# Performance work log

Measured on AMD Instinct MI355X. Metric: run time of the kernel, lower is better.

## Reference

```python
import jax, jax.numpy as jnp
import numpy as np

V, D, S, L, DK, DV, H, B = 32000, 1024, 1024, 4, 64, 64, 16, 4
DFF = 4 * D
EPS = 1e-5


def setup_inputs() -> dict:
    key = jax.random.key(0)
    ks = jax.random.split(key, 20)
    s = 0.02
    n = jax.random.normal
    return {
        "idx": jax.random.randint(ks[0], (B, S), 0, V, dtype=jnp.int32),
        "tok_emb": n(ks[1], (V, D), jnp.float32) * s,
        "pos_emb": n(ks[2], (S, D), jnp.float32) * s,
        "wq": n(ks[3], (L, H, D, DK), jnp.float32) * s,
        "wk": n(ks[4], (L, H, D, DK), jnp.float32) * s,
        "wv": n(ks[5], (L, H, D, DV), jnp.float32) * s,
        "wo": n(ks[6], (L, H * DV, D), jnp.float32) * s,
        "w1": n(ks[7], (L, D, DFF), jnp.float32) * s,
        "b1": jnp.zeros((L, DFF), jnp.float32),
        "w2": n(ks[8], (L, DFF, D), jnp.float32) * s,
        "b2": jnp.zeros((L, D), jnp.float32),
        "ln1_g": jnp.ones((L, D), jnp.float32),
        "ln1_b": jnp.zeros((L, D), jnp.float32),
        "ln2_g": jnp.ones((L, D), jnp.float32),
        "ln2_b": jnp.zeros((L, D), jnp.float32),
        "lnf_g": jnp.ones((D,), jnp.float32),
        "lnf_b": jnp.zeros((D,), jnp.float32),
        "lm_w": n(ks[9], (D, V), jnp.float32) * s,
        "lm_b": jnp.zeros((V,), jnp.float32),
    }


def _ln(x, g, b):
    mu = jnp.mean(x, axis=-1, keepdims=True)
    var = jnp.mean(jnp.square(x - mu), axis=-1, keepdims=True)
    return (x - mu) * jax.lax.rsqrt(var + EPS) * g + b


def _gpt(idx, tok_emb, pos_emb, wq, wk, wv, wo, w1, b1, w2, b2,
         ln1_g, ln1_b, ln2_g, ln2_b, lnf_g, lnf_b, lm_w, lm_b):
    x = tok_emb[idx] + pos_emb[None, :, :]          # [B,S,D]
    causal = jnp.tril(jnp.ones((S, S), bool))        # tril mask buffer
    scale = 1.0 / jnp.sqrt(jnp.asarray(DK, x.dtype))

    def block(x, p):
        wq, wk, wv, wo, w1, b1, w2, b2, g1, be1, g2, be2 = p
        h = _ln(x, g1, be1)
        Q = jnp.einsum('bsd,hdk->bhsk', h, wq)
        K = jnp.einsum('bsd,hdk->bhsk', h, wk)
        Vv = jnp.einsum('bsd,hdv->bhsv', h, wv)
        att = jnp.einsum('bhsk,bhtk->bhst', Q, K) * scale
        att = jnp.where(causal, att, -jnp.inf)
        att = jax.nn.softmax(att, axis=-1)
        o = jnp.einsum('bhst,bhtv->bshv', att, Vv).reshape(x.shape[0], S, H * DV)
        x = x + o @ wo
        h2 = _ln(x, g2, be2)
        x = x + jax.nn.relu(h2 @ w1 + b1) @ w2 + be2 * 0 + b2
        return x, None

    x, _ = jax.lax.scan(block, x, (wq, wk, wv, wo, w1, b1, w2, b2,
                                   ln1_g, ln1_b, ln2_g, ln2_b))
    x = _ln(x, lnf_g, lnf_b)
    logits = x @ lm_w + lm_b                          # [B,S,V]
    return logits


def reference(idx, tok_emb, pos_emb, wq, wk, wv, wo, w1, b1, w2, b2,
              ln1_g, ln1_b, ln2_g, ln2_b, lnf_g, lnf_b, lm_w, lm_b):
    return _gpt(idx, tok_emb, pos_emb, wq, wk, wv, wo, w1, b1, w2, b2,
                ln1_g, ln1_b, ln2_g, ln2_b, lnf_g, lnf_b, lm_w, lm_b)
```

## Files before the change

### kernel.cpp

```cpp
#include <hip/hip_runtime.h>
#include <hip/hip_bf16.h>

#define V_   32000
#define VP_  32768
#define D_   1024
#define S_   1024
#define L_   4
#define H_   16
#define B_   4
#define DFF_ 4096
#define M_   (B_*S_)

using bf_t = __hip_bfloat16;
typedef __bf16 bf16x8 __attribute__((ext_vector_type(8)));
typedef __bf16 bf16x4 __attribute__((ext_vector_type(4)));
typedef float  f32x4  __attribute__((ext_vector_type(4)));

#define AS1(p) ((__attribute__((address_space(1))) void*)(p))
#define AS3(p) ((__attribute__((address_space(3))) void*)(p))

__global__ __launch_bounds__(256) void k_transpose_bf16(
    const float* __restrict__ src, bf_t* __restrict__ dst,
    int R, int C, long srcS1, long srcS2, long dstS1, long dstS2, int n2)
{
  const int z  = blockIdx.z;
  const int z1 = z / n2, z2 = z % n2;
  src += (size_t)z1 * srcS1 + (size_t)z2 * srcS2;
  dst += (size_t)z1 * dstS1 + (size_t)z2 * dstS2;
  __shared__ float tile[32][33];
  const int c0 = blockIdx.x * 32, r0 = blockIdx.y * 32;
  const int lx = threadIdx.x, ly = threadIdx.y;
  #pragma unroll
  for (int i = 0; i < 32; i += 8)
    tile[ly + i][lx] = src[(size_t)(r0 + ly + i) * C + (c0 + lx)];
  __syncthreads();
  #pragma unroll
  for (int i = 0; i < 32; i += 8)
    dst[(size_t)(c0 + ly + i) * R + (r0 + lx)] = __float2bfloat16(tile[lx][ly + i]);
}

__global__ __launch_bounds__(256) void k_embed(
    const int* __restrict__ idx, const float* __restrict__ tok,
    const float* __restrict__ pos, float* __restrict__ x)
{
  const int row = blockIdx.x;
  const int s   = row & (S_ - 1);
  const int t   = idx[row];
  const float4* tr = (const float4*)(tok + (size_t)t * D_);
  const float4* pr = (const float4*)(pos + (size_t)s * D_);
  float4* xr = (float4*)(x + (size_t)row * D_);
  const int i = threadIdx.x;
  float4 a = tr[i], b = pr[i];
  xr[i] = make_float4(a.x + b.x, a.y + b.y, a.z + b.z, a.w + b.w);
}

__global__ __launch_bounds__(256) void k_ln(
    const float* __restrict__ x, const float* __restrict__ g,
    const float* __restrict__ bb, bf_t* __restrict__ out)
{
  __shared__ float red[8];
  const int row = blockIdx.x, tid = threadIdx.x;
  const float4 v = ((const float4*)(x + (size_t)row * D_))[tid];
  float s = v.x + v.y + v.z + v.w;
  #pragma unroll
  for (int o = 32; o > 0; o >>= 1) s += __shfl_down(s, o);
  if ((tid & 63) == 0) red[tid >> 6] = s;
  __syncthreads();
  const float mu = (red[0] + red[1] + red[2] + red[3]) * (1.f / D_);
  const float dx = v.x - mu, dy = v.y - mu, dz = v.z - mu, dw = v.w - mu;
  float ss = dx*dx + dy*dy + dz*dz + dw*dw;
  #pragma unroll
  for (int o = 32; o > 0; o >>= 1) ss += __shfl_down(ss, o);
  if ((tid & 63) == 0) red[4 + (tid >> 6)] = ss;
  __syncthreads();
  const float var = (red[4] + red[5] + red[6] + red[7]) * (1.f / D_);
  const float rs  = rsqrtf(var + 1e-5f);
  const float4 gv = ((const float4*)g)[tid];
  const float4 bv = ((const float4*)bb)[tid];
  const size_t base = (size_t)row * D_ + tid * 4;
  out[base + 0] = __float2bfloat16(dx * rs * gv.x + bv.x);
  out[base + 1] = __float2bfloat16(dy * rs * gv.y + bv.y);
  out[base + 2] = __float2bfloat16(dz * rs * gv.z + bv.z);
  out[base + 3] = __float2bfloat16(dw * rs * gv.w + bv.w);
}

__global__ __launch_bounds__(256) void k_combine_ln(
    float* __restrict__ x, const float* __restrict__ P, long pstride,
    const float* __restrict__ cbias,
    const float* __restrict__ g, const float* __restrict__ bb,
    bf_t* __restrict__ out)
{
  __shared__ float red[8];
  const int row = blockIdx.x, tid = threadIdx.x;
  const size_t i = (size_t)row * 256 + tid;
  float4 a = ((const float4*)x)[i];
  {
    const float4 p0 = ((const float4*)P)[i];
    const float4 p1 = ((const float4*)(P + pstride))[i];
    a.x += p0.x + p1.x; a.y += p0.y + p1.y;
    a.z += p0.z + p1.z; a.w += p0.w + p1.w;
  }
  if (cbias) {
    const float4 bv = ((const float4*)cbias)[tid];
    a.x += bv.x; a.y += bv.y; a.z += bv.z; a.w += bv.w;
  }
  ((float4*)x)[i] = a;
  float s = a.x + a.y + a.z + a.w;
  #pragma unroll
  for (int o = 32; o > 0; o >>= 1) s += __shfl_down(s, o);
  if ((tid & 63) == 0) red[tid >> 6] = s;
  __syncthreads();
  const float mu = (red[0] + red[1] + red[2] + red[3]) * (1.f / D_);
  const float dx = a.x - mu, dy = a.y - mu, dz = a.z - mu, dw = a.w - mu;
  float ss = dx*dx + dy*dy + dz*dz + dw*dw;
  #pragma unroll
  for (int o = 32; o > 0; o >>= 1) ss += __shfl_down(ss, o);
  if ((tid & 63) == 0) red[4 + (tid >> 6)] = ss;
  __syncthreads();
  const float var = (red[4] + red[5] + red[6] + red[7]) * (1.f / D_);
  const float rs  = rsqrtf(var + 1e-5f);
  const float4 gv = ((const float4*)g)[tid];
  const float4 bv = ((const float4*)bb)[tid];
  const size_t base = (size_t)row * D_ + tid * 4;
  out[base + 0] = __float2bfloat16(dx * rs * gv.x + bv.x);
  out[base + 1] = __float2bfloat16(dy * rs * gv.y + bv.y);
  out[base + 2] = __float2bfloat16(dz * rs * gv.z + bv.z);
  out[base + 3] = __float2bfloat16(dw * rs * gv.w + bv.w);
}

template<bool HAS_BIAS, bool RELU, bool OUT_BF16, bool NT, int PARTS>
__global__ __launch_bounds__(256) void k_gemm(
    const bf_t* __restrict__ A, const bf_t* __restrict__ Bt,
    float* outF, bf_t* outB,
    const float* __restrict__ bias,
    int N, int ld, int Klen, long pstride)
{
  __shared__ __bf16 As[2][128 * 64];
  __shared__ __bf16 Bs[2][128 * 64];
  const int tid  = threadIdx.x;
  const int lane = tid & 63, wid = tid >> 6;
  int bp = blockIdx.x, kh = 0;
  if (PARTS > 1) { const int T = gridDim.x / PARTS; kh = bp / T; bp %= T; }
  const int i  = bp >> 3;
  const int nt = (bp & 7) + 8 * (i >> 5);
  const int mt = i & 31;
  const int m0 = mt * 128;
  const int n0 = nt * 128;
  if (n0 >= N) return;
  const int kb = kh * Klen;
  f32x4 acc[4][4] = {};

  const int srow = lane >> 3;
  const int scol = ((lane & 7) ^ (lane >> 3)) * 8;
  const int mw = (wid >> 1) * 64, nw = (wid & 1) * 64;
  const int NTk = Klen >> 6;

  #pragma unroll
  for (int i2 = 0; i2 < 4; ++i2) {
    const int chunk = i2 * 4 + wid;
    const int r = chunk * 8 + srow;
    __builtin_amdgcn_global_load_lds(AS1(A  + (size_t)(m0 + r) * ld + kb + scol),
                                     AS3(&As[0][chunk * 512]), 16, 0, 0);
    __builtin_amdgcn_global_load_lds(AS1(Bt + (size_t)(n0 + r) * ld + kb + scol),
                                     AS3(&Bs[0][chunk * 512]), 16, 0, 0);
  }

  for (int t = 0; t < NTk; ++t) {
    __syncthreads();
    if (t + 1 < NTk) {
      const int kt = (t + 1) << 6;
      #pragma unroll
      for (int i2 = 0; i2 < 4; ++i2) {
        const int chunk = i2 * 4 + wid;
        const int r = chunk * 8 + srow;
        __builtin_amdgcn_global_load_lds(AS1(A  + (size_t)(m0 + r) * ld + kb + kt + scol),
                                         AS3(&As[(t + 1) & 1][chunk * 512]), 16, 0, 0);
        __builtin_amdgcn_global_load_lds(AS1(Bt + (size_t)(n0 + r) * ld + kb + kt + scol),
                                         AS3(&Bs[(t + 1) & 1][chunk * 512]), 16, 0, 0);
      }
    }
    const __bf16* Ab = As[t & 1];
    const __bf16* Bb = Bs[t & 1];
    #pragma unroll
    for (int kk = 0; kk < 2; ++kk) {
      const int ck = kk * 4 + (lane >> 4);
      bf16x8 af[4], bfr[4];
      #pragma unroll
      for (int mi = 0; mi < 4; ++mi) {
        const int r = mw + mi * 16 + (lane & 15);
        af[mi] = *(const bf16x8*)&Ab[r * 64 + ((ck ^ (r & 7)) * 8)];
      }
      #pragma unroll
      for (int ni = 0; ni < 4; ++ni) {
        const int r = nw + ni * 16 + (lane & 15);
        bfr[ni] = *(const bf16x8*)&Bb[r * 64 + ((ck ^ (r & 7)) * 8)];
      }
      #pragma unroll
      for (int mi = 0; mi < 4; ++mi)
        #pragma unroll
        for (int ni = 0; ni < 4; ++ni)
          acc[mi][ni] = __builtin_amdgcn_mfma_f32_16x16x32_bf16(af[mi], bfr[ni], acc[mi][ni], 0, 0, 0);
    }
  }

  float* outP = outF + (PARTS > 1 ? (size_t)kh * pstride : 0);
  const int cr = (lane >> 4) * 4, cc = lane & 15;
  #pragma unroll
  for (int mi = 0; mi < 4; ++mi) {
    #pragma unroll
    for (int ni = 0; ni < 4; ++ni) {
      const int col = n0 + nw + ni * 16 + cc;
      const float bv = HAS_BIAS ? bias[col] : 0.f;
      #pragma unroll
      for (int j = 0; j < 4; ++j) {
        const int row = m0 + mw + mi * 16 + cr + j;
        float v = acc[mi][ni][j] + bv;
        if (RELU)  v = fmaxf(v, 0.f);
        if (OUT_BF16) {
          outB[(size_t)row * N + col] = __float2bfloat16(v);
        } else if (NT) {
          __builtin_nontemporal_store(v, &outP[(size_t)row * N + col]);
        } else {
          outP[(size_t)row * N + col] = v;
        }
      }
    }
  }
}

__device__ __forceinline__ void stage256(
    const bf_t* __restrict__ A, const bf_t* __restrict__ Bt,
    int m0, int n0, int lda, int kt, int wid, int lane, __bf16* buf)
{
  #pragma unroll
  for (int p = 0; p < 4; ++p) {
    const int sb   = p * 512 + wid * 64;
    const int slot = sb + lane;
    const int row  = slot >> 3;
    const int c    = (slot & 7) ^ (row & 7);
    __builtin_amdgcn_global_load_lds(AS1(A  + (size_t)(m0 + row) * lda + kt + c * 8),
                                     AS3(buf + sb * 8), 16, 0, 0);
    __builtin_amdgcn_global_load_lds(AS1(Bt + (size_t)(n0 + row) * lda + kt + c * 8),
                                     AS3(buf + 16384 + sb * 8), 16, 0, 0);
  }
}

template<bool HAS_BIAS, bool RELU, bool OUT_BF16, bool NT, int MAP>
__global__ __launch_bounds__(512, 2) void k_gemm256(
    const bf_t* __restrict__ A, const bf_t* __restrict__ Bt,
    float* outF, bf_t* outB, const float* __restrict__ bias,
    int N, int Nvalid, int K)
{
  __shared__ __align__(16) __bf16 LDS[65536];
  const int tid = threadIdx.x, lane = tid & 63, wid = tid >> 6;
  int mt, nt;
  if (MAP == 0) { mt = blockIdx.x & 15; nt = blockIdx.x >> 4; }
  else {
    const int xcd = blockIdx.x & 7, i = blockIdx.x >> 3;
    mt = i & 15; nt = xcd + 8 * (i >> 4);
  }
  const int m0 = mt * 256, n0 = nt * 256;
  if (n0 >= Nvalid) return;
  const int wm = wid >> 2, wn = wid & 3;
  const int l4 = lane & 15, lhi = lane >> 4;

  f32x4 acc[8][4] = {};
  const int NTILES = K >> 6;

  stage256(A, Bt, m0, n0, K, 0,  wid, lane, LDS);
  stage256(A, Bt, m0, n0, K, 64, wid, lane, LDS + 32768);

  for (int t = 0; t < NTILES; ++t) {
    __bf16* buf = LDS + (t & 1) * 32768;
    if (t < NTILES - 1) asm volatile("s_waitcnt vmcnt(8)" ::: "memory");
    else                asm volatile("s_waitcnt vmcnt(0)" ::: "memory");
    __builtin_amdgcn_s_barrier();
    asm volatile("" ::: "memory");

    bf16x8 bq[4][2];
    #pragma unroll
    for (int ni = 0; ni < 4; ++ni) {
      const int r = wn * 64 + ni * 16 + l4;
      bq[ni][0] = *(const bf16x8*)&buf[16384 + r * 64 + ((lhi ^ (r & 7)) * 8)];
      bq[ni][1] = *(const bf16x8*)&buf[16384 + r * 64 + (((4 + lhi) ^ (r & 7)) * 8)];
    }
    bf16x8 aq[2][2][2];
    #pragma unroll
    for (int mi = 0; mi < 2; ++mi) {
      const int r = wm * 128 + mi * 16 + l4;
      aq[0][mi][0] = *(const bf16x8*)&buf[r * 64 + ((lhi ^ (r & 7)) * 8)];
      aq[0][mi][1] = *(const bf16x8*)&buf[r * 64 + (((4 + lhi) ^ (r & 7)) * 8)];
    }
    #pragma unroll
    for (int q = 0; q < 4; ++q) {
      if (q < 3) {
        #pragma unroll
        for (int mi = 0; mi < 2; ++mi) {
          const int r = wm * 128 + ((q + 1) * 2 + mi) * 16 + l4;
          aq[(q + 1) & 1][mi][0] = *(const bf16x8*)&buf[r * 64 + ((lhi ^ (r & 7)) * 8)];
          aq[(q + 1) & 1][mi][1] = *(const bf16x8*)&buf[r * 64 + (((4 + lhi) ^ (r & 7)) * 8)];
        }
      }
      #pragma unroll
      for (int mi = 0; mi < 2; ++mi)
        #pragma unroll
        for (int ni = 0; ni < 4; ++ni) {
          acc[q * 2 + mi][ni] = __builtin_amdgcn_mfma_f32_16x16x32_bf16(
              aq[q & 1][mi][0], bq[ni][0], acc[q * 2 + mi][ni], 0, 0, 0);
          acc[q * 2 + mi][ni] = __builtin_amdgcn_mfma_f32_16x16x32_bf16(
              aq[q & 1][mi][1], bq[ni][1], acc[q * 2 + mi][ni], 0, 0, 0);
        }
    }

    asm volatile("s_waitcnt lgkmcnt(0)" ::: "memory");
    __builtin_amdgcn_sched_barrier(0);
    __builtin_amdgcn_s_barrier();
    if (t + 2 < NTILES)
      stage256(A, Bt, m0, n0, K, (t + 2) * 64, wid, lane, buf);
  }

  float* slab = (float*)LDS + wid * 1088;
  float bval[4];
  if (HAS_BIAS) {
    #pragma unroll
    for (int ni = 0; ni < 4; ++ni) bval[ni] = bias[n0 + wn * 64 + ni * 16 + l4];
  }
  #pragma unroll
  for (int mi = 0; mi < 8; ++mi) {
    #pragma unroll
    for (int ni = 0; ni < 4; ++ni)
      #pragma unroll
      for (int j = 0; j < 4; ++j) {
        float v = acc[mi][ni][j];
        if (HAS_BIAS) v += bval[ni];
        if (RELU) v = fmaxf(v, 0.f);
        slab[(lhi * 4 + j) * 68 + ni * 16 + l4] = v;
      }
    const int grow0 = m0 + wm * 128 + mi * 16;
    const int ncol0 = n0 + wn * 64;
    #pragma unroll
    for (int q = 0; q < 4; ++q) {
      const int r16 = q * 4 + lhi;
      const f32x4 v = *(const f32x4*)&slab[r16 * 68 + l4 * 4];
      const size_t gaddr = (size_t)(grow0 + r16) * N + ncol0 + l4 * 4;
      if (OUT_BF16) {
        bf16x4 o4;
        o4[0] = (__bf16)v[0]; o4[1] = (__bf16)v[1];
        o4[2] = (__bf16)v[2]; o4[3] = (__bf16)v[3];
        *(bf16x4*)(outB + gaddr) = o4;
      } else if (NT) {
        __builtin_nontemporal_store(v, (f32x4*)(outF + gaddr));
      } else {
        *(f32x4*)(outF + gaddr) = v;
      }
    }
  }
}

__global__ __launch_bounds__(256) void k_attn_mfma(
    const bf_t* __restrict__ qkv, bf_t* __restrict__ o)
{
  __shared__ __bf16 Qs[64 * 64];
  __shared__ __bf16 Ks[64 * 64];
  __shared__ __bf16 Vt[64 * 64];
  __shared__ __bf16 Ps[4][16 * 64];

  const int qt = blockIdx.x, bh = blockIdx.y;
  const int b = bh >> 4, h = bh & 15;
  const int tid = threadIdx.x, lane = tid & 63, wid = tid >> 6;
  const int qbase = qt * 64;
  const int r0 = wid * 16;
  const int l4 = lane & 15, lhi = lane >> 4;

  #pragma unroll
  for (int p = 0; p < 2; ++p) {
    const int idx = p * 256 + tid;
    const int r = idx >> 3, c8 = idx & 7;
    const bf16x8 v = *(const bf16x8*)(qkv + (size_t)(b * S_ + qbase + r) * 3072 + h * 64 + c8 * 8);
    *(bf16x8*)&Qs[r * 64 + ((c8 ^ (r & 7)) * 8)] = v;
  }

  f32x4 oa[4];
  #pragma unroll
  for (int di = 0; di < 4; ++di) oa[di] = (f32x4){0.f, 0.f, 0.f, 0.f};
  float mrow = -1e30f, lrow = 0.f;

  const float SCL = 0.125f * 1.44269504089f;

  for (int kt = 0; kt <= qt; ++kt) {
    __syncthreads();
    #pragma unroll
    for (int p = 0; p < 2; ++p) {
      const int idx = p * 256 + tid;
      const int r = idx >> 3, c8 = idx & 7;
      const size_t gbase = (size_t)(b * S_ + kt * 64 + r) * 3072 + h * 64 + c8 * 8;
      const bf16x8 kv = *(const bf16x8*)(qkv + gbase + 1024);
      *(bf16x8*)&Ks[r * 64 + ((c8 ^ (r & 7)) * 8)] = kv;
      const bf16x8 vv = *(const bf16x8*)(qkv + gbase + 2048);
      #pragma unroll
      for (int i = 0; i < 8; ++i) {
        const int d = c8 * 8 + i;
        Vt[d * 64 + (((r >> 3) ^ i ^ c8) * 8) + (r & 7)] = vv[i];
      }
    }
    __syncthreads();

    f32x4 s[4];
    #pragma unroll
    for (int ni = 0; ni < 4; ++ni) s[ni] = (f32x4){0.f, 0.f, 0.f, 0.f};
    const int qr = r0 + l4;
    __builtin_amdgcn_s_setprio(1);
    #pragma unroll
    for (int kk = 0; kk < 2; ++kk) {
      const int ck = kk * 4 + lhi;
      const bf16x8 bq = *(const bf16x8*)&Qs[qr * 64 + ((ck ^ (qr & 7)) * 8)];
      #pragma unroll
      for (int ni = 0; ni < 4; ++ni) {
        const int t = ni * 16 + l4;
        const bf16x8 ak = *(const bf16x8*)&Ks[t * 64 + ((ck ^ (t & 7)) * 8)];
        s[ni] = __builtin_amdgcn_mfma_f32_16x16x32_bf16(ak, bq, s[ni], 0, 0, 0);
      }
    }
    __builtin_amdgcn_s_setprio(0);

    #pragma unroll
    for (int ni = 0; ni < 4; ++ni)
      #pragma unroll
      for (int j = 0; j < 4; ++j)
        s[ni][j] *= SCL;
    if (kt == qt) {
      #pragma unroll
      for (int ni = 0; ni < 4; ++ni)
        #pragma unroll
        for (int j = 0; j < 4; ++j)
          if (ni * 16 + lhi * 4 + j > r0 + l4) s[ni][j] = -1e30f;
    }

    float mloc = -1e30f;
    #pragma unroll
    for (int ni = 0; ni < 4; ++ni)
      #pragma unroll
      for (int j = 0; j < 4; ++j) mloc = fmaxf(mloc, s[ni][j]);
    mloc = fmaxf(mloc, __shfl_xor(mloc, 16));
    mloc = fmaxf(mloc, __shfl_xor(mloc, 32));
    float cscale = 1.f;
    if (!__all(mloc <= mrow + 8.f)) {
      const float mnew = fmaxf(mrow, mloc);
      cscale = exp2f(mrow - mnew);
      #pragma unroll
      for (int j = 0; j < 4; ++j) {
        const float cj = __shfl(cscale, lhi * 4 + j);
        #pragma unroll
        for (int di = 0; di < 4; ++di) oa[di][j] *= cj;
      }
      mrow = mnew;
    }
    float ssum = 0.f;
    #pragma unroll
    for (int ni = 0; ni < 4; ++ni)
      #pragma unroll
      for (int j = 0; j < 4; ++j) {
        const float pv = exp2f(s[ni][j] - mrow);
        s[ni][j] = pv;
        ssum += pv;
      }
    ssum += __shfl_xor(ssum, 16);
    ssum += __shfl_xor(ssum, 32);
    lrow = lrow * cscale + ssum;

    #pragma unroll
    for (int ni = 0; ni < 4; ++ni)
      #pragma unroll
      for (int j = 0; j < 4; ++j) {
        const int c = ni * 16 + lhi * 4 + j;
        Ps[wid][l4 * 64 + (((c >> 3) ^ (l4 & 7)) * 8) + (c & 7)] = (__bf16)s[ni][j];
      }

    __builtin_amdgcn_s_setprio(1);
    #pragma unroll
    for (int kk = 0; kk < 2; ++kk) {
      const int ck = kk * 4 + lhi;
      const bf16x8 ap = *(const bf16x8*)&Ps[wid][l4 * 64 + ((ck ^ (l4 & 7)) * 8)];
      #pragma unroll
      for (int di = 0; di < 4; ++di) {
        const int d = di * 16 + l4;
        const bf16x8 bv = *(const bf16x8*)&Vt[d * 64 + ((ck ^ (d & 7) ^ ((d >> 3) & 7)) * 8)];
        oa[di] = __builtin_amdgcn_mfma_f32_16x16x32_bf16(ap, bv, oa[di], 0, 0, 0);
      }
    }
    __builtin_amdgcn_s_setprio(0);
  }

  #pragma unroll
  for (int j = 0; j < 4; ++j) {
    const float lj = __shfl(lrow, lhi * 4 + j);
    const float inv = 1.f / lj;
    const size_t row = (size_t)(b * S_) + qbase + r0 + lhi * 4 + j;
    #pragma unroll
    for (int di = 0; di < 4; ++di)
      o[row * 1024 + h * 64 + di * 16 + l4] = __float2bfloat16(oa[di][j] * inv);
  }
}

extern "C" void kernel_launch(void* const* d_in, const int* in_sizes, int n_in,
                              void* d_out, int out_size, void* d_ws, size_t ws_size,
                              hipStream_t stream)
{
  (void)in_sizes; (void)n_in; (void)out_size; (void)ws_size;
  const int*   idx  = (const int*)  d_in[0];
  const float* tok  = (const float*)d_in[1];
  const float* pos  = (const float*)d_in[2];
  const float* wq   = (const float*)d_in[3];
  const float* wk   = (const float*)d_in[4];
  const float* wv   = (const float*)d_in[5];
  const float* wo   = (const float*)d_in[6];
  const float* w1   = (const float*)d_in[7];
  const float* b1   = (const float*)d_in[8];
  const float* w2   = (const float*)d_in[9];
  const float* b2   = (const float*)d_in[10];
  const float* ln1g = (const float*)d_in[11];
  const float* ln1b = (const float*)d_in[12];
  const float* ln2g = (const float*)d_in[13];
  const float* ln2b = (const float*)d_in[14];
  const float* lnfg = (const float*)d_in[15];
  const float* lnfb = (const float*)d_in[16];
  const float* lmw  = (const float*)d_in[17];
  const float* lmb  = (const float*)d_in[18];
  float* out = (float*)d_out;

  char* ws = (char*)d_ws;
  size_t off = 0;
  auto alloc = [&](size_t bytes) {
    void* p = ws + off; off += (bytes + 255) & ~(size_t)255; return p;
  };
  bf_t*  qkvw = (bf_t*) alloc((size_t)L_ * 3072 * 1024 * 2);
  bf_t*  wot  = (bf_t*) alloc((size_t)L_ * 1024 * 1024 * 2);
  bf_t*  w1t  = (bf_t*) alloc((size_t)L_ * 4096 * 1024 * 2);
  bf_t*  w2t  = (bf_t*) alloc((size_t)L_ * 1024 * 4096 * 2);
  bf_t*  lmwt = (bf_t*) alloc((size_t)VP_ * 1024 * 2);
  float* x    = (float*)alloc((size_t)M_ * D_ * 4);
  bf_t*  hbuf = (bf_t*) alloc((size_t)M_ * D_ * 2);
  bf_t*  qkvb = (bf_t*) alloc((size_t)M_ * 3072 * 2);
  bf_t*  attb = (bf_t*) alloc((size_t)M_ * D_ * 2);
  bf_t*  ffnb = (bf_t*) alloc((size_t)M_ * DFF_ * 2);
  float* PpartO = (float*)ffnb;
  float* PpartF = (float*)qkvb;
  const long PSTRIDE = (long)M_ * 1024;

  const dim3 tb(32, 8);
  k_transpose_bf16<<<dim3(2, 32, L_*H_), tb, 0, stream>>>(
      wq, qkvw + 0 * 1024 * 1024, D_, 64,
      (long)H_*D_*64, (long)D_*64, (long)3*1024*1024, (long)64*1024, H_);
  k_transpose_bf16<<<dim3(2, 32, L_*H_), tb, 0, stream>>>(
      wk, qkvw + 1 * 1024 * 1024, D_, 64,
      (long)H_*D_*64, (long)D_*64, (long)3*1024*1024, (long)64*1024, H_);
  k_transpose_bf16<<<dim3(2, 32, L_*H_), tb, 0, stream>>>(
      wv, qkvw + 2 * 1024 * 1024, D_, 64,
      (long)H_*D_*64, (long)D_*64, (long)3*1024*1024, (long)64*1024, H_);
  k_transpose_bf16<<<dim3(32, 32, L_), tb, 0, stream>>>(
      wo, wot, 1024, 1024, (long)1024*1024, 0, (long)1024*1024, 0, 1);
  k_transpose_bf16<<<dim3(128, 32, L_), tb, 0, stream>>>(
      w1, w1t, 1024, 4096, (long)1024*4096, 0, (long)1024*4096, 0, 1);
  k_transpose_bf16<<<dim3(32, 128, L_), tb, 0, stream>>>(
      w2, w2t, 4096, 1024, (long)4096*1024, 0, (long)4096*1024, 0, 1);
  k_transpose_bf16<<<dim3(1000, 32, 1), tb, 0, stream>>>(
      lmw, lmwt, 1024, V_, 0, 0, 0, 0, 1);

  k_embed<<<M_, 256, 0, stream>>>(idx, tok, pos, x);
  k_ln<<<M_, 256, 0, stream>>>(x, ln1g, ln1b, hbuf);

  for (int l = 0; l < L_; ++l) {
    k_gemm256<false, false, true, false, 0><<<12 * 16, 512, 0, stream>>>(
        hbuf, qkvw + (size_t)l * 3072 * 1024, nullptr, qkvb, nullptr,
        3072, 3072, 1024);
    k_attn_mfma<<<dim3(S_ / 64, B_ * H_), 256, 0, stream>>>(qkvb, attb);
    k_gemm<false, false, false, false, 2><<<2 * 8 * 32, 256, 0, stream>>>(
        attb, wot + (size_t)l * 1024 * 1024, PpartO, nullptr, nullptr,
        1024, 1024, 512, PSTRIDE);
    k_combine_ln<<<M_, 256, 0, stream>>>(
        x, PpartO, PSTRIDE, nullptr, ln2g + l * D_, ln2b + l * D_, hbuf);
    k_gemm256<true, true, true, false, 0><<<16 * 16, 512, 0, stream>>>(
        hbuf, w1t + (size_t)l * 4096 * 1024, nullptr, ffnb, b1 + l * DFF_,
        4096, 4096, 1024);
    k_gemm<false, false, false, false, 2><<<2 * 8 * 32, 256, 0, stream>>>(
        ffnb, w2t + (size_t)l * 1024 * 4096, PpartF, nullptr, nullptr,
        1024, 4096, 2048, PSTRIDE);
    const float* ng = (l < L_ - 1) ? (ln1g + (l + 1) * D_) : lnfg;
    const float* nb = (l < L_ - 1) ? (ln1b + (l + 1) * D_) : lnfb;
    k_combine_ln<<<M_, 256, 0, stream>>>(
        x, PpartF, PSTRIDE, b2 + l * D_, ng, nb, hbuf);
  }

  k_gemm256<true, false, false, true, 1><<<16 * 128, 512, 0, stream>>>(
      hbuf, lmwt, out, nullptr, lmb,
      V_, V_, 1024);
}
```

Baseline: 1.384 ms.

## Interleave half-tile async loads with MFMA phases in 256x256 GEMM

Restructures the GEMM main loop so global-to-LDS staging is split into four half-tile loads, each issued inside one of the four MFMA sub-phases, with barriers and s_setprio around the MFMA bursts. The aim is to hide load latency by overlapping it finely with compute instead of issuing all loads at the end of each K-step. Launch bounds drop from 2 to 1 blocks per CU, which gives more registers but removes inter-block overlap. The added per-phase barriers and a tricky buffer-reuse schedule, where A is prefetched one tile ahead into the other buffer, risk stalls or races.

New measurement: 1.318 ms. -4.7%, faster.

```diff
diff --git a/kernel.cpp b/kernel.cpp
--- a/kernel.cpp
+++ b/kernel.cpp
@@ -228,25 +228,23 @@
   }
 }
 
-__device__ __forceinline__ void stage256(
-    const bf_t* __restrict__ A, const bf_t* __restrict__ Bt,
-    int m0, int n0, int lda, int kt, int wid, int lane, __bf16* buf)
-{
-  #pragma unroll
-  for (int p = 0; p < 4; ++p) {
-    const int sb   = p * 512 + wid * 64;
-    const int slot = sb + lane;
-    const int row  = slot >> 3;
-    const int c    = (slot & 7) ^ (row & 7);
-    __builtin_amdgcn_global_load_lds(AS1(A  + (size_t)(m0 + row) * lda + kt + c * 8),
-                                     AS3(buf + sb * 8), 16, 0, 0);
-    __builtin_amdgcn_global_load_lds(AS1(Bt + (size_t)(n0 + row) * lda + kt + c * 8),
-                                     AS3(buf + 16384 + sb * 8), 16, 0, 0);
+__device__ __forceinline__ void stage_half(
+    const bf_t* __restrict__ src, int row0, int ld, int kt,
+    int tid, __bf16* lds_base)
+{
+  #pragma unroll
+  for (int p = 0; p < 2; ++p) {
+    const int sb   = p * 512 + (tid & ~63);
+    const int slot = sb + (tid & 63);
+    const int r = slot >> 3;
+    const int c = (slot & 7) ^ (r & 7);
+    __builtin_amdgcn_global_load_lds(AS1(src + (size_t)(row0 + r) * ld + kt + c * 8),
+                                     AS3(lds_base + sb * 8), 16, 0, 0);
   }
 }
 
 template<bool HAS_BIAS, bool RELU, bool OUT_BF16, bool NT, int MAP>
-__global__ __launch_bounds__(512, 2) void k_gemm256(
+__global__ __launch_bounds__(512, 1) void k_gemm256(
     const bf_t* __restrict__ A, const bf_t* __restrict__ Bt,
     float* outF, bf_t* outB, const float* __restrict__ bias,
     int N, int Nvalid, int K)
@@ -267,56 +265,71 @@
   f32x4 acc[8][4] = {};
   const int NTILES = K >> 6;
 
-  stage256(A, Bt, m0, n0, K, 0,  wid, lane, LDS);
-  stage256(A, Bt, m0, n0, K, 64, wid, lane, LDS + 32768);
+  stage_half(A,  m0,       K, 0,  tid, LDS + 0 * 8192);
+  stage_half(A,  m0 + 128, K, 0,  tid, LDS + 1 * 8192);
+  stage_half(Bt, n0,       K, 0,  tid, LDS + 32768 + 0 * 8192);
+  stage_half(Bt, n0 + 128, K, 0,  tid, LDS + 32768 + 1 * 8192);
+  stage_half(A,  m0,       K, 64, tid, LDS + 2 * 8192);
+  stage_half(A,  m0 + 128, K, 64, tid, LDS + 3 * 8192);
+  stage_half(Bt, n0,       K, 64, tid, LDS + 32768 + 2 * 8192);
+  stage_half(Bt, n0 + 128, K, 64, tid, LDS + 32768 + 3 * 8192);
+  asm volatile("s_waitcnt vmcnt(8)" ::: "memory");
+  __builtin_amdgcn_s_barrier();
+  asm volatile("" ::: "memory");
 
   for (int t = 0; t < NTILES; ++t) {
-    __bf16* buf = LDS + (t & 1) * 32768;
-    if (t < NTILES - 1) asm volatile("s_waitcnt vmcnt(8)" ::: "memory");
-    else                asm volatile("s_waitcnt vmcnt(0)" ::: "memory");
-    __builtin_amdgcn_s_barrier();
-    asm volatile("" ::: "memory");
-
+    const int d = t & 1;
+    const __bf16* Abase = LDS + (d * 2 + wm) * 8192;
+    const __bf16* Bbase = LDS + 32768 + (d * 2 + (wn >> 1)) * 8192;
     bf16x8 bq[4][2];
     #pragma unroll
-    for (int ni = 0; ni < 4; ++ni) {
-      const int r = wn * 64 + ni * 16 + l4;
-      bq[ni][0] = *(const bf16x8*)&buf[16384 + r * 64 + ((lhi ^ (r & 7)) * 8)];
-      bq[ni][1] = *(const bf16x8*)&buf[16384 + r * 64 + (((4 + lhi) ^ (r & 7)) * 8)];
-    }
-    bf16x8 aq[2][2][2];
-    #pragma unroll
-    for (int mi = 0; mi < 2; ++mi) {
-      const int r = wm * 128 + mi * 16 + l4;
-      aq[0][mi][0] = *(const bf16x8*)&buf[r * 64 + ((lhi ^ (r & 7)) * 8)];
-      aq[0][mi][1] = *(const bf16x8*)&buf[r * 64 + (((4 + lhi) ^ (r & 7)) * 8)];
-    }
-    #pragma unroll
     for (int q = 0; q < 4; ++q) {
-      if (q < 3) {
-        #pragma unroll
-        for (int mi = 0; mi < 2; ++mi) {
-          const int r = wm * 128 + ((q + 1) * 2 + mi) * 16 + l4;
-          aq[(q + 1) & 1][mi][0] = *(const bf16x8*)&buf[r * 64 + ((lhi ^ (r & 7)) * 8)];
-          aq[(q + 1) & 1][mi][1] = *(const bf16x8*)&buf[r * 64 + (((4 + lhi) ^ (r & 7)) * 8)];
-        }
-      }
-      #pragma unroll
-      for (int mi = 0; mi < 2; ++mi)
+      if (q == 0) {
         #pragma unroll
         for (int ni = 0; ni < 4; ++ni) {
-          acc[q * 2 + mi][ni] = __builtin_amdgcn_mfma_f32_16x16x32_bf16(
-              aq[q & 1][mi][0], bq[ni][0], acc[q * 2 + mi][ni], 0, 0, 0);
-          acc[q * 2 + mi][ni] = __builtin_amdgcn_mfma_f32_16x16x32_bf16(
-              aq[q & 1][mi][1], bq[ni][1], acc[q * 2 + mi][ni], 0, 0, 0);
+          const int r = (wn & 1) * 64 + ni * 16 + l4;
+          bq[ni][0] = *(const bf16x8*)&Bbase[r * 64 + ((lhi ^ (r & 7)) * 8)];
+          bq[ni][1] = *(const bf16x8*)&Bbase[r * 64 + (((4 + lhi) ^ (r & 7)) * 8)];
         }
-    }
-
-    asm volatile("s_waitcnt lgkmcnt(0)" ::: "memory");
-    __builtin_amdgcn_sched_barrier(0);
-    __builtin_amdgcn_s_barrier();
-    if (t + 2 < NTILES)
-      stage256(A, Bt, m0, n0, K, (t + 2) * 64, wid, lane, buf);
+      }
+      bf16x8 aq[2][2];
+      #pragma unroll
+      for (int mi2 = 0; mi2 < 2; ++mi2) {
+        const int r = (q * 2 + mi2) * 16 + l4;
+        aq[mi2][0] = *(const bf16x8*)&Abase[r * 64 + ((lhi ^ (r & 7)) * 8)];
+        aq[mi2][1] = *(const bf16x8*)&Abase[r * 64 + (((4 + lhi) ^ (r & 7)) * 8)];
+      }
+      if (q == 0 && t >= 1 && t + 1 < NTILES)
+        stage_half(A, m0, K, (t + 1) * 64, tid,
+                   LDS + (((t + 1) & 1) * 2 + 0) * 8192);
+      if (q == 1 && t >= 1 && t + 1 < NTILES)
+        stage_half(A, m0 + 128, K, (t + 1) * 64, tid,
+                   LDS + (((t + 1) & 1) * 2 + 1) * 8192);
+      if (q == 2 && t + 2 < NTILES)
+        stage_half(Bt, n0, K, (t + 2) * 64, tid,
+                   LDS + 32768 + (((t + 2) & 1) * 2 + 0) * 8192);
+      if (q == 3 && t + 2 < NTILES)
+        stage_half(Bt, n0 + 128, K, (t + 2) * 64, tid,
+                   LDS + 32768 + (((t + 2) & 1) * 2 + 1) * 8192);
+      __builtin_amdgcn_s_barrier();
+      __builtin_amdgcn_s_setprio(1);
+      #pragma unroll
+      for (int mi2 = 0; mi2 < 2; ++mi2)
+        #pragma unroll
+        for (int ni = 0; ni < 4; ++ni) {
+          acc[q * 2 + mi2][ni] = __builtin_amdgcn_mfma_f32_16x16x32_bf16(
+              aq[mi2][0], bq[ni][0], acc[q * 2 + mi2][ni], 0, 0, 0);
+          acc[q * 2 + mi2][ni] = __builtin_amdgcn_mfma_f32_16x16x32_bf16(
+              aq[mi2][1], bq[ni][1], acc[q * 2 + mi2][ni], 0, 0, 0);
+        }
+      __builtin_amdgcn_s_setprio(0);
+      if (q == 3) {
+        if (t + 2 < NTILES) asm volatile("s_waitcnt vmcnt(4)" ::: "memory");
+        else                asm volatile("s_waitcnt vmcnt(0)" ::: "memory");
+      }
+      __builtin_amdgcn_s_barrier();
+      asm volatile("" ::: "memory");
+    }
   }
 
   float* slab = (float*)LDS + wid * 1088;
```
